# Performance work log

Measured on AMD Instinct MI355X. Metric: run time of the kernel, lower is better.

## Reference

```python
import jax, jax.numpy as jnp
import numpy as np

B, P, G, CIN, COUT, WD, K3 = 4, 32768, 64, 128, 128, 512, 27
N = B * P


def _build_kernel_map(rng):
    # random sparse occupancy per batch instance on a G^3 grid
    flat = np.stack([rng.choice(G ** 3, size=P, replace=False) for _ in range(B)])  # [B,P]
    b = np.repeat(np.arange(B), P).astype(np.int64)
    f = flat.reshape(-1).astype(np.int64)
    x = f // (G * G); y = (f // G) % G; z = f % G
    keys = b * (G ** 3) + f
    order = np.argsort(keys); skeys = keys[order]
    offsets = [(dx, dy, dz) for dx in (-1, 0, 1) for dy in (-1, 0, 1) for dz in (-1, 0, 1)]
    in_idx = np.full((K3, N), N, np.int32)   # N is a dummy (zero-feature) row
    out_idx = np.full((K3, N), N, np.int32)  # N is a dummy (discarded) output row
    for k, (dx, dy, dz) in enumerate(offsets):
        nx, ny, nz = x + dx, y + dy, z + dz
        inb = (nx >= 0) & (nx < G) & (ny >= 0) & (ny < G) & (nz >= 0) & (nz < G)
        nkey = b * (G ** 3) + (nx * G + ny) * G + nz
        pos = np.clip(np.searchsorted(skeys, nkey), 0, N - 1)
        found = inb & (skeys[pos] == nkey)
        cnt = int(found.sum())
        in_idx[k, :cnt] = order[pos[found]]
        out_idx[k, :cnt] = np.nonzero(found)[0]
    return b.astype(np.int32), in_idx, out_idx


def setup_inputs() -> dict:
    rng = np.random.default_rng(0)
    batch_idx, in_idx, out_idx = _build_kernel_map(rng)
    key = jax.random.key(0)
    k1, k2, k3, k4 = jax.random.split(key, 4)
    return {
        "x_feat": jax.random.normal(k1, (N, CIN), jnp.float32),
        "w": jax.random.normal(k2, (B, WD), jnp.float32),
        "affine_weight": jax.random.normal(k3, (CIN, WD), jnp.float32),
        "affine_bias": jnp.ones((CIN,), jnp.float32),  # bias_init=1
        "conv_weight": jax.random.normal(k4, (COUT, CIN, 3, 3, 3), jnp.float32),
        "conv_bias": jnp.zeros((COUT,), jnp.float32),
        "magnitude_ema": jnp.ones((), jnp.float32),
        "batch_idx": jnp.asarray(batch_idx),
        "in_idx": jnp.asarray(in_idx),
        "out_idx": jnp.asarray(out_idx),
    }


def reference(x_feat, w, affine_weight, affine_bias, conv_weight, conv_bias,
              magnitude_ema, batch_idx, in_idx, out_idx):
    n, cin = x_feat.shape
    cout = conv_weight.shape[0]
    # affine: FullyConnectedLayer with weight_gain = 1/sqrt(in_features), bias_init=1
    styles = w @ (affine_weight * (1.0 / np.sqrt(affine_weight.shape[1]))).T + affine_bias  # [B,Cin]
    # demodulate pre-normalization
    wn = conv_weight * jax.lax.rsqrt(jnp.mean(jnp.square(conv_weight), axis=(1, 2, 3, 4), keepdims=True))
    sn = styles * jax.lax.rsqrt(jnp.mean(jnp.square(styles)))
    sw = wn[None] * sn[:, None, :, None, None, None]              # [B,Cout,Cin,3,3,3]
    dcoefs = jax.lax.rsqrt(jnp.sum(jnp.square(sw), axis=(2, 3, 4, 5)) + 1e-8)  # [B,Cout]
    # non-fused modconv: per-point style modulation (index_select by batch column)
    xmod = x_feat * sn[batch_idx]                                 # [N,Cin]
    xpad = jnp.concatenate([xmod, jnp.zeros((1, cin), xmod.dtype)], axis=0)
    # sparse conv: gather -> GEMM -> scatter-add per kernel offset
    wk = jnp.transpose(wn.reshape(cout, cin, K3), (2, 1, 0))      # [27,Cin,Cout]
    out = jnp.zeros((n + 1, cout), x_feat.dtype)
    for k in range(K3):
        out = out.at[out_idx[k]].add(xpad[in_idx[k]] @ wk[k])
    out = out[:n]
    out = out * dcoefs[batch_idx]                                 # demodulation per point
    out = out * jax.lax.rsqrt(magnitude_ema)                      # input_gain
    # fused bias + leaky relu + gain + clamp
    out = out + conv_bias
    out = jnp.where(out < 0, 0.2 * out, out) * np.sqrt(2.0)
    return jnp.clip(out, -256.0, 256.0)
```

## Files before the change

kernel.cpp:

```cpp
#include <hip/hip_runtime.h>
#include <stdint.h>

#define NPTS 131072
#define CINC 128
#define COUTC 128
#define WDIM 512
#define K3 27

typedef float f32x4 __attribute__((ext_vector_type(4)));
typedef __bf16 bf16x8 __attribute__((ext_vector_type(8)));

__device__ __forceinline__ unsigned short f2bf(float x){
  union { float f; uint32_t u; } v; v.f = x;
  uint32_t u = v.u;
  uint32_t r = (u + 0x7fffu + ((u >> 16) & 1u)) >> 16;
  return (unsigned short)r;
}

__global__ void k_styles(const float* __restrict__ w, const float* __restrict__ aw,
                         const float* __restrict__ ab, float* __restrict__ sn){
  __shared__ float red[512];
  int t = threadIdx.x;
  int b = t >> 7, c = t & 127;
  const float* wr = w + b * WDIM;
  const float* ar = aw + c * WDIM;
  float s = 0.f;
  for (int d = 0; d < WDIM; d++) s += wr[d] * ar[d];
  s = s * 0.04419417382415922f + ab[c];
  red[t] = s * s;
  __syncthreads();
  for (int off = 256; off > 0; off >>= 1){
    if (t < off) red[t] += red[t + off];
    __syncthreads();
  }
  float ms = red[0] * (1.0f / 512.0f);
  sn[t] = s * rsqrtf(ms);
}

__global__ void k_wnorm(const float* __restrict__ cw, float* __restrict__ wnorm){
  __shared__ float red[256];
  int co = blockIdx.x, t = threadIdx.x;
  const float* p = cw + co * 3456;
  float s = 0.f;
  for (int i = t; i < 3456; i += 256){ float v = p[i]; s += v * v; }
  red[t] = s; __syncthreads();
  for (int off = 128; off > 0; off >>= 1){
    if (t < off) red[t] += red[t + off];
    __syncthreads();
  }
  if (t == 0) wnorm[co] = rsqrtf(red[0] * (1.0f / 3456.0f));
}

__global__ void k_dcoefs(const float* __restrict__ cw, const float* __restrict__ sn,
                         const float* __restrict__ wnorm, const float* __restrict__ mag,
                         float* __restrict__ dco2){
  int blk = blockIdx.x;
  int b = blk >> 7, co = blk & 127;
  int lane = threadIdx.x;
  float sum = 0.f;
  for (int cin = lane; cin < CINC; cin += 64){
    float s = sn[b * CINC + cin]; float s2 = s * s;
    const float* p = cw + co * 3456 + cin * 27;
    float c2 = 0.f;
    for (int k = 0; k < 27; k++){ float v = p[k]; c2 += v * v; }
    sum += c2 * s2;
  }
  for (int off = 32; off > 0; off >>= 1) sum += __shfl_down(sum, off, 64);
  if (lane == 0){
    float wn2 = wnorm[co]; wn2 *= wn2;
    dco2[blk] = rsqrtf(sum * wn2 + 1e-8f) * rsqrtf(mag[0]);
  }
}

__global__ void k_bpack(const float* __restrict__ cw, const float* __restrict__ wnorm,
                        unsigned short* __restrict__ bpack){
  int blk = blockIdx.x;
  int k = blk >> 5; int rem = blk & 31; int kk = rem >> 3;
  int lane = threadIdx.x; int q = lane >> 4, m = lane & 15;
  int grp = rem & 7;
  int cout = grp * 16 + m;
  float ws = wnorm[cout];
  unsigned short* dst = bpack + (blk * 64 + lane) * 8;
  for (int j = 0; j < 8; j++){
    int cin = kk * 32 + q * 8 + j;
    dst[j] = f2bf(cw[cout * 3456 + cin * 27 + k] * ws);
  }
}

__global__ void k_xmod(const float* __restrict__ x, const float* __restrict__ sn,
                       const int* __restrict__ bidx, unsigned short* __restrict__ xpad){
  int gid = blockIdx.x * 256 + threadIdx.x;
  const int total = (NPTS + 1) * 32;
  if (gid >= total) return;
  int n = gid >> 5;
  int c4 = (gid & 31) * 4;
  unsigned short o0, o1, o2, o3;
  if (n < NPTS){
    int b = bidx[n];
    const float* xr = x + (size_t)n * CINC + c4;
    const float* sr = sn + b * CINC + c4;
    o0 = f2bf(xr[0] * sr[0]); o1 = f2bf(xr[1] * sr[1]);
    o2 = f2bf(xr[2] * sr[2]); o3 = f2bf(xr[3] * sr[3]);
  } else { o0 = o1 = o2 = o3 = 0; }
  *(ushort4*)(xpad + (size_t)n * CINC + c4) = make_ushort4(o0, o1, o2, o3);
}

__global__ void k_invinit(int* __restrict__ invT){
  int j = blockIdx.x * 256 + threadIdx.x;
  int k = blockIdx.y;
  invT[k * NPTS + j] = NPTS;
}

__global__ void k_invscat(const int* __restrict__ out_idx, const int* __restrict__ in_idx,
                          int* __restrict__ invT){
  int j = blockIdx.x * 256 + threadIdx.x;
  int k = blockIdx.y;
  int o = out_idx[k * NPTS + j];
  if (o < NPTS) invT[k * NPTS + o] = in_idx[k * NPTS + j];
}

__global__ __launch_bounds__(512, 4) void k_conv(
    const unsigned short* __restrict__ xpad,
    const unsigned short* __restrict__ bpack,
    const int* __restrict__ invT,
    const float* __restrict__ dco2,
    const float* __restrict__ cbias,
    const int* __restrict__ bidx,
    float* __restrict__ out){
  __shared__ __align__(16) unsigned short Ash[128 * 128];
  __shared__ __align__(16) unsigned short Bsh[16384];
  int t = threadIdx.x;
  int wave = t >> 6, lane = t & 63;
  int wm = wave >> 1, wn = wave & 1;
  int q = lane >> 4, m16 = lane & 15;
  int base_pt = blockIdx.x * 128;

  f32x4 acc[2][4];
  #pragma unroll
  for (int i = 0; i < 2; i++)
    #pragma unroll
    for (int j = 0; j < 4; j++) acc[i][j] = (f32x4){0.f, 0.f, 0.f, 0.f};

  for (int k = 0; k < K3; k++){
    __syncthreads();
    {
      const int4* src = (const int4*)(bpack + k * 16384);
      int4* dstB = (int4*)Bsh;
      #pragma unroll
      for (int i = 0; i < 4; i++){
        int c = i * 512 + t;
        dstB[c] = src[c];
      }
    }
    {
      const int* invk = invT + k * NPTS + base_pt;
      #pragma unroll
      for (int i = 0; i < 4; i++){
        int chunk = i * 512 + t;
        int row = chunk >> 4, c = chunk & 15;
        int inv = invk[row];
        int4 v = *(const int4*)(xpad + (size_t)inv * CINC + c * 8);
        *(int4*)(Ash + row * 128 + ((c ^ row) & 15) * 8) = v;
      }
    }
    __syncthreads();
    #pragma unroll
    for (int kk = 0; kk < 4; kk++){
      int cA = (kk * 4 + q) ^ m16;
      bf16x8 a0 = *(const bf16x8*)(Ash + (wm * 32 + m16) * 128 + (cA & 15) * 8);
      bf16x8 a1 = *(const bf16x8*)(Ash + (wm * 32 + 16 + m16) * 128 + (cA & 15) * 8);
      #pragma unroll
      for (int jn = 0; jn < 4; jn++){
        bf16x8 b = *(const bf16x8*)(Bsh + ((kk * 8 + wn * 4 + jn) * 64 + lane) * 8);
        acc[0][jn] = __builtin_amdgcn_mfma_f32_16x16x32_bf16(a0, b, acc[0][jn], 0, 0, 0);
        acc[1][jn] = __builtin_amdgcn_mfma_f32_16x16x32_bf16(a1, b, acc[1][jn], 0, 0, 0);
      }
    }
  }

  const float S2 = 1.41421356237309515f;
  #pragma unroll
  for (int i = 0; i < 2; i++){
    #pragma unroll
    for (int r = 0; r < 4; r++){
      int row = wm * 32 + i * 16 + q * 4 + r;
      int n = base_pt + row;
      int b = bidx[n];
      const float* dc = dco2 + b * COUTC;
      float* orow = out + (size_t)n * COUTC;
      #pragma unroll
      for (int jn = 0; jn < 4; jn++){
        int col = wn * 64 + jn * 16 + m16;
        float v = acc[i][jn][r] * dc[col] + cbias[col];
        v = (v < 0.f ? 0.2f * v : v) * S2;
        v = fminf(fmaxf(v, -256.f), 256.f);
        orow[col] = v;
      }
    }
  }
}

extern "C" void kernel_launch(void* const* d_in, const int* in_sizes, int n_in,
                              void* d_out, int out_size, void* d_ws, size_t ws_size,
                              hipStream_t stream){
  const float* x   = (const float*)d_in[0];
  const float* w   = (const float*)d_in[1];
  const float* aw  = (const float*)d_in[2];
  const float* ab  = (const float*)d_in[3];
  const float* cw  = (const float*)d_in[4];
  const float* cb  = (const float*)d_in[5];
  const float* mag = (const float*)d_in[6];
  const int* bidx    = (const int*)d_in[7];
  const int* in_idx  = (const int*)d_in[8];
  const int* out_idx = (const int*)d_in[9];
  float* out = (float*)d_out;
  char* ws = (char*)d_ws;

  float* sn    = (float*)(ws + 0);
  float* dco2  = (float*)(ws + 2048);
  float* wnorm = (float*)(ws + 4096);
  unsigned short* bpack = (unsigned short*)(ws + 8192);
  unsigned short* xpad  = (unsigned short*)(ws + 892928);
  int* invT    = (int*)(ws + 34447616);

  k_styles<<<1, 512, 0, stream>>>(w, aw, ab, sn);
  k_wnorm<<<128, 256, 0, stream>>>(cw, wnorm);
  k_dcoefs<<<512, 64, 0, stream>>>(cw, sn, wnorm, mag, dco2);
  k_bpack<<<864, 64, 0, stream>>>(cw, wnorm, bpack);
  k_xmod<<<16385, 256, 0, stream>>>(x, sn, bidx, xpad);
  dim3 gi(512, 27);
  k_invinit<<<gi, 256, 0, stream>>>(invT);
  k_invscat<<<gi, 256, 0, stream>>>(out_idx, in_idx, invT);
  k_conv<<<1024, 512, 0, stream>>>(xpad, bpack, invT, dco2, cb, bidx, out);
}
```

Before: 340.7 us.

## Double-buffer gathered A tiles via async global-to-LDS loads and parallelize prep kernels

The sparse conv kernel now gathers the A tile for the next kernel offset with global_load_lds into a second LDS buffer while MFMAs run on the current one. The XOR swizzle moves to the source address, and there is one barrier per offset instead of two. The B weight fragments are read straight from global/L2 instead of being staged in LDS. Weight preprocessing is also reworked: norm, bpack and per-(cout,cin) squared sums are fused into one kernel, the style dot products are spread across waves, and xmod uses float4 loads. The aim is to hide gather latency and cut the serial prep work, at the cost of more global traffic for B and reliance on L2 hits.

```diff
diff --git a/kernel.cpp b/kernel.cpp
--- a/kernel.cpp
+++ b/kernel.cpp
@@ -10,6 +10,10 @@
 typedef float f32x4 __attribute__((ext_vector_type(4)));
 typedef __bf16 bf16x8 __attribute__((ext_vector_type(8)));
 
+#define GLOAD_LDS16(g, l) \
+  __builtin_amdgcn_global_load_lds((const __attribute__((address_space(1))) void*)(g), \
+                                   (__attribute__((address_space(3))) void*)(l), 16, 0, 0)
+
 __device__ __forceinline__ unsigned short f2bf(float x){
   union { float f; uint32_t u; } v; v.f = x;
   uint32_t u = v.u;
@@ -17,73 +21,73 @@
   return (unsigned short)r;
 }
 
-__global__ void k_styles(const float* __restrict__ w, const float* __restrict__ aw,
-                         const float* __restrict__ ab, float* __restrict__ sn){
+__global__ void k_styles_dot(const float* __restrict__ w, const float* __restrict__ aw,
+                             const float* __restrict__ ab, float* __restrict__ styles){
+  int wave = threadIdx.x >> 6, lane = threadIdx.x & 63;
+  int blk = blockIdx.x * 4 + wave;
+  int b = blk >> 7, c = blk & 127;
+  const float4* wr = (const float4*)(w + b * WDIM);
+  const float4* ar = (const float4*)(aw + c * WDIM);
+  float4 w0 = wr[lane * 2], w1 = wr[lane * 2 + 1];
+  float4 a0 = ar[lane * 2], a1 = ar[lane * 2 + 1];
+  float s = w0.x * a0.x + w0.y * a0.y + w0.z * a0.z + w0.w * a0.w
+          + w1.x * a1.x + w1.y * a1.y + w1.z * a1.z + w1.w * a1.w;
+  for (int off = 32; off > 0; off >>= 1) s += __shfl_down(s, off, 64);
+  if (lane == 0) styles[blk] = s * 0.04419417382415922f + ab[c];
+}
+
+__global__ void k_snorm(const float* __restrict__ styles, float* __restrict__ sn){
   __shared__ float red[512];
   int t = threadIdx.x;
-  int b = t >> 7, c = t & 127;
-  const float* wr = w + b * WDIM;
-  const float* ar = aw + c * WDIM;
-  float s = 0.f;
-  for (int d = 0; d < WDIM; d++) s += wr[d] * ar[d];
-  s = s * 0.04419417382415922f + ab[c];
+  float s = styles[t];
   red[t] = s * s;
   __syncthreads();
   for (int off = 256; off > 0; off >>= 1){
     if (t < off) red[t] += red[t + off];
     __syncthreads();
   }
-  float ms = red[0] * (1.0f / 512.0f);
-  sn[t] = s * rsqrtf(ms);
-}
-
-__global__ void k_wnorm(const float* __restrict__ cw, float* __restrict__ wnorm){
-  __shared__ float red[256];
-  int co = blockIdx.x, t = threadIdx.x;
-  const float* p = cw + co * 3456;
-  float s = 0.f;
-  for (int i = t; i < 3456; i += 256){ float v = p[i]; s += v * v; }
-  red[t] = s; __syncthreads();
-  for (int off = 128; off > 0; off >>= 1){
-    if (t < off) red[t] += red[t + off];
+  sn[t] = s * rsqrtf(red[0] * (1.0f / 512.0f));
+}
+
+__global__ void k_prep_w(const float* __restrict__ cw, float* __restrict__ wnorm,
+                         float* __restrict__ vmat, unsigned short* __restrict__ bpack){
+  __shared__ float red[128];
+  int co = blockIdx.x, cin = threadIdx.x;
+  const float* p = cw + co * 3456 + cin * 27;
+  float r[27];
+  float v = 0.f;
+  #pragma unroll
+  for (int k = 0; k < 27; k++){ r[k] = p[k]; v += r[k] * r[k]; }
+  vmat[co * 128 + cin] = v;
+  red[cin] = v;
+  __syncthreads();
+  for (int off = 64; off > 0; off >>= 1){
+    if (cin < off) red[cin] += red[cin + off];
     __syncthreads();
   }
-  if (t == 0) wnorm[co] = rsqrtf(red[0] * (1.0f / 3456.0f));
-}
-
-__global__ void k_dcoefs(const float* __restrict__ cw, const float* __restrict__ sn,
-                         const float* __restrict__ wnorm, const float* __restrict__ mag,
-                         float* __restrict__ dco2){
-  int blk = blockIdx.x;
-  int b = blk >> 7, co = blk & 127;
-  int lane = threadIdx.x;
-  float sum = 0.f;
-  for (int cin = lane; cin < CINC; cin += 64){
-    float s = sn[b * CINC + cin]; float s2 = s * s;
-    const float* p = cw + co * 3456 + cin * 27;
-    float c2 = 0.f;
-    for (int k = 0; k < 27; k++){ float v = p[k]; c2 += v * v; }
-    sum += c2 * s2;
-  }
+  float wn_s = rsqrtf(red[0] * (1.0f / 3456.0f));
+  if (cin == 0) wnorm[co] = wn_s;
+  int grp = co >> 4, m = co & 15;
+  int kk = cin >> 5, q = (cin >> 3) & 3, j = cin & 7;
+  #pragma unroll
+  for (int k = 0; k < 27; k++){
+    int idx = ((k * 32 + kk * 8 + grp) * 64 + q * 16 + m) * 8 + j;
+    bpack[idx] = f2bf(r[k] * wn_s);
+  }
+}
+
+__global__ void k_dcoefs2(const float* __restrict__ vmat, const float* __restrict__ sn,
+                          const float* __restrict__ wnorm, const float* __restrict__ mag,
+                          float* __restrict__ dco2){
+  int wave = threadIdx.x >> 6, lane = threadIdx.x & 63;
+  int pair = blockIdx.x * 8 + wave;
+  int b = pair >> 7, co = pair & 127;
+  float s0 = sn[b * 128 + lane], s1 = sn[b * 128 + 64 + lane];
+  float sum = vmat[co * 128 + lane] * s0 * s0 + vmat[co * 128 + 64 + lane] * s1 * s1;
   for (int off = 32; off > 0; off >>= 1) sum += __shfl_down(sum, off, 64);
   if (lane == 0){
-    float wn2 = wnorm[co]; wn2 *= wn2;
-    dco2[blk] = rsqrtf(sum * wn2 + 1e-8f) * rsqrtf(mag[0]);
-  }
-}
-
-__global__ void k_bpack(const float* __restrict__ cw, const float* __restrict__ wnorm,
-                        unsigned short* __restrict__ bpack){
-  int blk = blockIdx.x;
-  int k = blk >> 5; int rem = blk & 31; int kk = rem >> 3;
-  int lane = threadIdx.x; int q = lane >> 4, m = lane & 15;
-  int grp = rem & 7;
-  int cout = grp * 16 + m;
-  float ws = wnorm[cout];
-  unsigned short* dst = bpack + (blk * 64 + lane) * 8;
-  for (int j = 0; j < 8; j++){
-    int cin = kk * 32 + q * 8 + j;
-    dst[j] = f2bf(cw[cout * 3456 + cin * 27 + k] * ws);
+    float wn = wnorm[co];
+    dco2[pair] = rsqrtf(sum * wn * wn + 1e-8f) * rsqrtf(mag[0]);
   }
 }
 
@@ -97,10 +101,10 @@
   unsigned short o0, o1, o2, o3;
   if (n < NPTS){
     int b = bidx[n];
-    const float* xr = x + (size_t)n * CINC + c4;
-    const float* sr = sn + b * CINC + c4;
-    o0 = f2bf(xr[0] * sr[0]); o1 = f2bf(xr[1] * sr[1]);
-    o2 = f2bf(xr[2] * sr[2]); o3 = f2bf(xr[3] * sr[3]);
+    float4 xv = *(const float4*)(x + (size_t)n * CINC + c4);
+    float4 sv = *(const float4*)(sn + b * CINC + c4);
+    o0 = f2bf(xv.x * sv.x); o1 = f2bf(xv.y * sv.y);
+    o2 = f2bf(xv.z * sv.z); o3 = f2bf(xv.w * sv.w);
   } else { o0 = o1 = o2 = o3 = 0; }
   *(ushort4*)(xpad + (size_t)n * CINC + c4) = make_ushort4(o0, o1, o2, o3);
 }
@@ -127,8 +131,7 @@
     const float* __restrict__ cbias,
     const int* __restrict__ bidx,
     float* __restrict__ out){
-  __shared__ __align__(16) unsigned short Ash[128 * 128];
-  __shared__ __align__(16) unsigned short Bsh[16384];
+  __shared__ __align__(16) unsigned short Ash[2 * 128 * 128];
   int t = threadIdx.x;
   int wave = t >> 6, lane = t & 63;
   int wm = wave >> 1, wn = wave & 1;
@@ -141,37 +144,33 @@
     #pragma unroll
     for (int j = 0; j < 4; j++) acc[i][j] = (f32x4){0.f, 0.f, 0.f, 0.f};
 
+  auto prefetch = [&](int k, int bufsel){
+    const int* invk = invT + k * NPTS + base_pt;
+    unsigned short* Ab = Ash + bufsel * (128 * 128);
+    #pragma unroll
+    for (int i = 0; i < 4; i++){
+      int chunk = i * 512 + t;
+      int row = chunk >> 4, c = chunk & 15;
+      int inv = invk[row];
+      const unsigned short* src = xpad + (size_t)inv * CINC + ((c ^ row) & 15) * 8;
+      GLOAD_LDS16(src, Ab + chunk * 8);
+    }
+  };
+
+  prefetch(0, 0);
   for (int k = 0; k < K3; k++){
     __syncthreads();
-    {
-      const int4* src = (const int4*)(bpack + k * 16384);
-      int4* dstB = (int4*)Bsh;
-      #pragma unroll
-      for (int i = 0; i < 4; i++){
-        int c = i * 512 + t;
-        dstB[c] = src[c];
-      }
-    }
-    {
-      const int* invk = invT + k * NPTS + base_pt;
-      #pragma unroll
-      for (int i = 0; i < 4; i++){
-        int chunk = i * 512 + t;
-        int row = chunk >> 4, c = chunk & 15;
-        int inv = invk[row];
-        int4 v = *(const int4*)(xpad + (size_t)inv * CINC + c * 8);
-        *(int4*)(Ash + row * 128 + ((c ^ row) & 15) * 8) = v;
-      }
-    }
-    __syncthreads();
+    if (k + 1 < K3) prefetch(k + 1, (k + 1) & 1);
+    const unsigned short* Ab = Ash + (k & 1) * (128 * 128);
+    const unsigned short* Bg = bpack + k * 16384;
     #pragma unroll
     for (int kk = 0; kk < 4; kk++){
-      int cA = (kk * 4 + q) ^ m16;
-      bf16x8 a0 = *(const bf16x8*)(Ash + (wm * 32 + m16) * 128 + (cA & 15) * 8);
-      bf16x8 a1 = *(const bf16x8*)(Ash + (wm * 32 + 16 + m16) * 128 + (cA & 15) * 8);
+      int cA = ((kk * 4 + q) ^ m16) & 15;
+      bf16x8 a0 = *(const bf16x8*)(Ab + (wm * 32 + m16) * 128 + cA * 8);
+      bf16x8 a1 = *(const bf16x8*)(Ab + (wm * 32 + 16 + m16) * 128 + cA * 8);
       #pragma unroll
       for (int jn = 0; jn < 4; jn++){
-        bf16x8 b = *(const bf16x8*)(Bsh + ((kk * 8 + wn * 4 + jn) * 64 + lane) * 8);
+        bf16x8 b = *(const bf16x8*)(Bg + ((kk * 8 + wn * 4 + jn) * 64 + lane) * 8);
         acc[0][jn] = __builtin_amdgcn_mfma_f32_16x16x32_bf16(a0, b, acc[0][jn], 0, 0, 0);
         acc[1][jn] = __builtin_amdgcn_mfma_f32_16x16x32_bf16(a1, b, acc[1][jn], 0, 0, 0);
       }
@@ -216,17 +215,19 @@
   float* out = (float*)d_out;
   char* ws = (char*)d_ws;
 
-  float* sn    = (float*)(ws + 0);
-  float* dco2  = (float*)(ws + 2048);
-  float* wnorm = (float*)(ws + 4096);
-  unsigned short* bpack = (unsigned short*)(ws + 8192);
-  unsigned short* xpad  = (unsigned short*)(ws + 892928);
-  int* invT    = (int*)(ws + 34447616);
-
-  k_styles<<<1, 512, 0, stream>>>(w, aw, ab, sn);
-  k_wnorm<<<128, 256, 0, stream>>>(cw, wnorm);
-  k_dcoefs<<<512, 64, 0, stream>>>(cw, sn, wnorm, mag, dco2);
-  k_bpack<<<864, 64, 0, stream>>>(cw, wnorm, bpack);
+  float* styles = (float*)(ws + 0);
+  float* sn     = (float*)(ws + 2048);
+  float* wnorm  = (float*)(ws + 4096);
+  float* dco2   = (float*)(ws + 4608);
+  float* vmat   = (float*)(ws + 8192);
+  unsigned short* bpack = (unsigned short*)(ws + 73728);
+  unsigned short* xpad  = (unsigned short*)(ws + 958464);
+  int* invT     = (int*)(ws + 34513152);
+
+  k_prep_w<<<128, 128, 0, stream>>>(cw, wnorm, vmat, bpack);
+  k_styles_dot<<<128, 256, 0, stream>>>(w, aw, ab, styles);
+  k_snorm<<<1, 512, 0, stream>>>(styles, sn);
+  k_dcoefs2<<<64, 512, 0, stream>>>(vmat, sn, wnorm, mag, dco2);
   k_xmod<<<16385, 256, 0, stream>>>(x, sn, bidx, xpad);
   dim3 gi(512, 27);
   k_invinit<<<gi, 256, 0, stream>>>(invT);
```

New measurement: 325.8 us. 1.05x faster.
